# Optimization experiments

Measured on AMD Instinct MI355X. Metric: run time of the kernel, lower is better.

The kernel has to match this reference:

```python
import jax, jax.numpy as jnp
import numpy as np

B, T, NI, NH, NO = 32, 2048, 1, 512, 1


def setup_inputs() -> dict:
    key = jax.random.key(0)
    ks = jax.random.split(key, 7)
    x = jax.random.normal(ks[0], (B, T, NI), dtype=jnp.float32)
    # torch code draws h_0 ~ U[-1,1) once and tiles over batch; here per-batch uniform
    h_0 = jax.random.uniform(ks[1], (B, NH), dtype=jnp.float32) * 2.0 - 1.0
    w_input_std = 1.0 / np.sqrt(NH)
    W_ih = jax.random.normal(ks[2], (NH, NI), dtype=jnp.float32) * w_input_std
    prob_c = 0.1
    w_hidden_std = 1.5 / np.sqrt(prob_c * NH)
    mask = jax.random.bernoulli(ks[3], prob_c, (NH, NH)).astype(jnp.float32)
    W_hh = jax.random.normal(ks[4], (NH, NH), dtype=jnp.float32) * w_hidden_std * mask
    W_hz = jax.random.normal(ks[5], (NO, NH), dtype=jnp.float32) * w_input_std
    W_zh = jax.random.uniform(ks[6], (NH, NO), dtype=jnp.float32, minval=-1.0, maxval=1.0)
    return {"x": x, "h_0": h_0, "W_ih": W_ih, "W_hh": W_hh, "W_hz": W_hz, "W_zh": W_zh}


def reference(x, h_0, W_ih, W_hh, W_hz, W_zh):
    dt, tau = 0.001, 0.01
    alpha = dt / tau  # 0.1
    # precompute input projection for all timesteps: [T, B, NH]
    x_proj = jnp.einsum('bti,hi->tbh', x, W_ih)

    def step(carry, xp_t):
        h_prev, z_prev = carry  # [B,NH], [B,NO]
        h_transfer = jnp.tanh(h_prev)
        dhdt = -h_prev + h_transfer @ W_hh.T + xp_t + z_prev @ W_zh.T
        h_t = h_prev + alpha * dhdt
        z_t = jnp.tanh(h_t) @ W_hz.T
        return (h_t, z_t), (h_t, z_t)

    z0 = jnp.tanh(h_0) @ W_hz.T
    _, (h, z) = jax.lax.scan(step, (h_0, z0), x_proj)
    # scan stacks time first -> [T,B,*]; transpose to [B,T,*]
    return jnp.swapaxes(z, 0, 1), jnp.swapaxes(h, 0, 1)
```

## Files before the change

kernel.cpp:

```cpp
#include <hip/hip_runtime.h>


#define NH   512
#define TT   2048
#define BB   32
#define PAD  96
#define SENT 64

__global__ __launch_bounds__(512) void count_nnz(
    const float* __restrict__ Whh, int* __restrict__ nnz) {
  const int wib  = threadIdx.x >> 6;
  const int lane = threadIdx.x & 63;
  const int row  = blockIdx.x * 8 + wib;
  const float* wrow = Whh + (size_t)row * NH;
  int cnt = 0;
  for (int c = 0; c < NH / 64; ++c)
    cnt += __popcll(__ballot(wrow[c * 64 + lane] != 0.0f));
  if (lane == 0) nnz[row] = cnt;
}

__global__ __launch_bounds__(512) void sort_rows(
    const int* __restrict__ nnz, int* __restrict__ perm) {
  __shared__ int nl[NH];
  const int j = threadIdx.x;
  const int my = nnz[j];
  nl[j] = my;
  __syncthreads();
  int r = 0;
  const int4* p4 = (const int4*)nl;
  for (int i = 0; i < NH / 4; ++i) {
    int4 v = p4[i];
    const int base = i * 4;
    r += (v.x > my) || (v.x == my && base + 0 < j);
    r += (v.y > my) || (v.y == my && base + 1 < j);
    r += (v.z > my) || (v.z == my && base + 2 < j);
    r += (v.w > my) || (v.w == my && base + 3 < j);
  }
  perm[r] = j;
}

__global__ __launch_bounds__(64) void build_schedule(
    const float* __restrict__ Whh, const int* __restrict__ perm,
    float* __restrict__ vals, unsigned* __restrict__ offs,
    int* __restrict__ cntw) {
  __shared__ int claim[2][32];
  const int lane = threadIdx.x;
  const int wid  = blockIdx.x;
  const int p    = wid * 64 + lane;
  const int half = lane >> 5;
  const int home = lane & 31;
  const int row  = perm[p];
  const float* wrow = Whh + (size_t)row * NH;

  unsigned occ32[16];
  int remaining = 0;
  unsigned nonempty = 0;
  #pragma unroll
  for (int r = 0; r < 16; ++r) {
    unsigned lo = 0, hi = 0;
    #pragma unroll
    for (int m = 0; m < 16; ++m) {
      lo |= (wrow[(2 * r)     + 32 * m] != 0.f) ? (1u << m) : 0u;
      hi |= (wrow[(2 * r + 1) + 32 * m] != 0.f) ? (1u << m) : 0u;
    }
    occ32[r] = lo | (hi << 16);
    remaining += __popc(lo) + __popc(hi);
    if (lo) nonempty |= 1u << (2 * r);
    if (hi) nonempty |= 1u << (2 * r + 1);
  }

  int s = 0;
  while (__ballot(remaining > 0) != 0ull) {
    claim[half][home] = SENT;
    __builtin_amdgcn_wave_barrier();

    const bool force = (remaining > 0) && ((PAD - s) <= remaining);
    bool placed = false;
    int  mybank = 0;
    unsigned excl = 0;

    for (int round = 0; round < 8; ++round) {
      unsigned cand = (placed || remaining == 0) ? 0u : (nonempty & ~excl);
      bool want = cand != 0u;
      int bl = 0;
      if (want) {
        unsigned rot = home ? ((cand >> home) | (cand << (32 - home))) : cand;
        bl = (home + __ffs(rot) - 1) & 31;
      }
      if (__ballot(want) == 0ull) break;
      bool win = false;
      if (want) {
        if (force) {
          win = true;
        } else {
          atomicMin(&claim[half][bl], lane);
          __builtin_amdgcn_wave_barrier();
          int c = ((volatile int*)claim[half])[bl];
          if (c == lane) { win = true; ((volatile int*)claim[half])[bl] = -1; }
          else           excl |= 1u << bl;
        }
      }
      __builtin_amdgcn_wave_barrier();
      if (win) { placed = true; mybank = bl; }
    }

    float v = 0.f; unsigned col = 0u;
    if (placed) {
      #pragma unroll
      for (int r = 0; r < 16; ++r) {
        if (r == (mybank >> 1)) {
          unsigned w   = occ32[r];
          unsigned m16 = (mybank & 1) ? (w >> 16) : (w & 0xFFFFu);
          int m = __ffs(m16) - 1;
          col = (unsigned)(mybank + 32 * m);
          unsigned nm = m16 & (m16 - 1u);
          occ32[r] = (mybank & 1) ? ((w & 0x0000FFFFu) | (nm << 16))
                                  : ((w & 0xFFFF0000u) | nm);
          if (nm == 0u) nonempty &= ~(1u << mybank);
        }
      }
      v = wrow[col];
      --remaining;
    }
    vals[s * NH + p] = v;
    offs[s * NH + p] = col;
    ++s;
  }
  if (lane == 0) cntw[wid] = s;
  for (int e = s; e < PAD; ++e) {
    vals[e * NH + p] = 0.f;
    offs[e * NH + p] = 0u;
  }
}

template <int CTRL, int RM>
__device__ __forceinline__ float dppadd(float v) {
  int t = __builtin_amdgcn_update_dpp(0, __float_as_int(v), CTRL, RM, 0xF, true);
  return v + __int_as_float(t);
}
__device__ __forceinline__ float wave_sum_lane63(float v) {
  v = dppadd<0xB1,  0xF>(v);
  v = dppadd<0x4E,  0xF>(v);
  v = dppadd<0x141, 0xF>(v);
  v = dppadd<0x140, 0xF>(v);
  v = dppadd<0x142, 0xA>(v);
  v = dppadd<0x143, 0xC>(v);
  return v;
}

#define ESN_STEP(T_RD, T_WR, RWR, SIDX)                                      \
  {                                                                          \
    float d0 = 0.f, d1 = 0.f, d2 = 0.f, d3 = 0.f;                            \
    _Pragma("unroll")                                                        \
    for (int e = 0; e < PAD; e += 8) {                                       \
      if (e < cw) {                                                          \
        d0 = fmaf(wval[e + 0], T_RD[cidx[e + 0]], d0);                       \
        d1 = fmaf(wval[e + 1], T_RD[cidx[e + 1]], d1);                       \
        d2 = fmaf(wval[e + 2], T_RD[cidx[e + 2]], d2);                       \
        d3 = fmaf(wval[e + 3], T_RD[cidx[e + 3]], d3);                       \
        d0 = fmaf(wval[e + 4], T_RD[cidx[e + 4]], d0);                       \
        d1 = fmaf(wval[e + 5], T_RD[cidx[e + 5]], d1);                       \
        d2 = fmaf(wval[e + 6], T_RD[cidx[e + 6]], d2);                       \
        d3 = fmaf(wval[e + 7], T_RD[cidx[e + 7]], d3);                       \
      }                                                                      \
    }                                                                        \
    float dot  = (d0 + d1) + (d2 + d3);                                      \
    float xp   = x_lds[SIDX] * w_ih;                                         \
    float dhdt = ((dot - h) + xp) + z_prev * w_zh;                           \
    float hn   = h + 0.1f * dhdt;                                            \
    float thn  = tanhf(hn);                                                  \
    T_WR[row] = thn;                                                         \
    oh[(SIDX) * NH + row] = hn;                                              \
    float pzs = wave_sum_lane63(thn * w_hz);                                 \
    if (lane == 63) red[RWR][wid] = pzs;                                     \
    asm volatile("s_waitcnt lgkmcnt(0)\n\ts_barrier" ::: "memory");          \
    float4 r0 = *(const float4*)&red[RWR][0];                                \
    float4 r1 = *(const float4*)&red[RWR][4];                                \
    float z = ((r0.x + r0.y) + (r0.z + r0.w)) + ((r1.x + r1.y) + (r1.z + r1.w)); \
    if (p == 0) oz[SIDX] = z;                                                \
    z_prev = z; h = hn;                                                      \
  }

__global__ __launch_bounds__(512, 2) void esn_steps(
    const float* __restrict__ x,   const float* __restrict__ h0,
    const float* __restrict__ Wih, const float* __restrict__ Whz,
    const float* __restrict__ Wzh, const float* __restrict__ vals,
    const unsigned* __restrict__ offs, const int* __restrict__ perm,
    const int* __restrict__ cntw, float* __restrict__ out) {
  __shared__ float t_lds[2][NH];
  __shared__ float x_lds[TT];
  __shared__ __align__(16) float red[2][8];

  const int p    = threadIdx.x;
  const int b    = blockIdx.x;
  const int lane = p & 63;
  const int wid  = p >> 6;
  const int row  = perm[p];

  float* t0 = t_lds[0];
  float* t1 = t_lds[1];

  for (int i = p; i < TT; i += NH) x_lds[i] = x[(size_t)b * TT + i];

  int cw = __builtin_amdgcn_readfirstlane((cntw[wid] + 7) & ~7);

  float    wval[PAD];
  unsigned cidx[PAD];
  #pragma unroll
  for (int e = 0; e < PAD; ++e) wval[e] = vals[e * NH + p];
  #pragma unroll
  for (int e = 0; e < PAD; ++e) cidx[e] = offs[e * NH + p];

  const float w_ih = Wih[row];
  const float w_hz = Whz[row];
  const float w_zh = Wzh[row];
  float h = h0[(size_t)b * NH + row];

  float* oz = out + (size_t)b * TT;
  float* oh = out + (size_t)BB * TT + (size_t)b * TT * NH;

  float th0 = tanhf(h);
  t0[row] = th0;
  float pz = wave_sum_lane63(th0 * w_hz);
  if (lane == 63) red[0][wid] = pz;
  __syncthreads();
  float4 i0 = *(const float4*)&red[0][0];
  float4 i1 = *(const float4*)&red[0][4];
  float z_prev = ((i0.x + i0.y) + (i0.z + i0.w)) + ((i1.x + i1.y) + (i1.z + i1.w));

  for (int s = 0; s < TT; s += 2) {
    ESN_STEP(t0, t1, 1, s);
    ESN_STEP(t1, t0, 0, s + 1);
  }
}

extern "C" void kernel_launch(void* const* d_in, const int* in_sizes, int n_in,
                              void* d_out, int out_size, void* d_ws,
                              size_t ws_size, hipStream_t stream) {
  const float* x   = (const float*)d_in[0];
  const float* h0  = (const float*)d_in[1];
  const float* Wih = (const float*)d_in[2];
  const float* Whh = (const float*)d_in[3];
  const float* Whz = (const float*)d_in[4];
  const float* Wzh = (const float*)d_in[5];
  float* out = (float*)d_out;

  float*    vals = (float*)d_ws;
  unsigned* offs = (unsigned*)(vals + PAD * NH);
  int*      nnz  = (int*)(offs + PAD * NH);
  int*      perm = nnz + NH;
  int*      cntw = perm + NH;

  hipLaunchKernelGGL(count_nnz, dim3(NH / 8), dim3(512), 0, stream, Whh, nnz);
  hipLaunchKernelGGL(sort_rows, dim3(1), dim3(512), 0, stream, nnz, perm);
  hipLaunchKernelGGL(build_schedule, dim3(8), dim3(64), 0, stream,
                     Whh, perm, vals, offs, cntw);
  hipLaunchKernelGGL(esn_steps, dim3(BB), dim3(512), 0, stream,
                     x, h0, Wih, Whz, Wzh, vals, offs, perm, cntw, out);
}
```

Baseline: 2.846 ms.

## Rework bank-conflict slot scheduler, use fast tanh, byte offsets, and pin registers

The slot-assignment loop that packs sparse W_hh entries into bank-conflict-free columns now uses atomicMax with a priority key favouring lanes with the most remaining entries, allows more rounds, and bounds the outer loop by PAD. The forced placement is also moved after the rounds. In the recurrent step, tanhf is replaced by an exp/rcp-based approximation, and LDS gather indices are precomputed as byte offsets so no shift is needed per access. Empty asm constraints pin the first 80 weight/index pairs in VGPRs to stop the compiler spilling or rematerialising them. The fast tanh gives up some accuracy, and the bounded scheduler loop could drop entries if it fails to place them all.

```diff
diff --git a/kernel.cpp b/kernel.cpp
--- a/kernel.cpp
+++ b/kernel.cpp
@@ -5,7 +5,7 @@
 #define TT   2048
 #define BB   32
 #define PAD  96
-#define SENT 64
+#define PIN  80
 
 __global__ __launch_bounds__(512) void count_nnz(
     const float* __restrict__ Whh, int* __restrict__ nnz) {
@@ -70,16 +70,16 @@
   }
 
   int s = 0;
-  while (__ballot(remaining > 0) != 0ull) {
-    claim[half][home] = SENT;
+  while (__ballot(remaining > 0) != 0ull && s < PAD) {
+    claim[half][home] = 0;
     __builtin_amdgcn_wave_barrier();
 
-    const bool force = (remaining > 0) && ((PAD - s) <= remaining);
     bool placed = false;
     int  mybank = 0;
     unsigned excl = 0;
-
-    for (int round = 0; round < 8; ++round) {
+    const int key = (remaining << 8) | (lane + 1);
+
+    for (int round = 0; round < 12; ++round) {
       unsigned cand = (placed || remaining == 0) ? 0u : (nonempty & ~excl);
       bool want = cand != 0u;
       int bl = 0;
@@ -88,20 +88,23 @@
         bl = (home + __ffs(rot) - 1) & 31;
       }
       if (__ballot(want) == 0ull) break;
-      bool win = false;
+      if (want) atomicMax(&claim[half][bl], key);
+      __builtin_amdgcn_wave_barrier();
       if (want) {
-        if (force) {
-          win = true;
+        int c = ((volatile int*)claim[half])[bl];
+        if (c == key) {
+          placed = true; mybank = bl;
+          ((volatile int*)claim[half])[bl] = 0x7FFFFFFF;
         } else {
-          atomicMin(&claim[half][bl], lane);
-          __builtin_amdgcn_wave_barrier();
-          int c = ((volatile int*)claim[half])[bl];
-          if (c == lane) { win = true; ((volatile int*)claim[half])[bl] = -1; }
-          else           excl |= 1u << bl;
+          excl |= 1u << bl;
         }
       }
       __builtin_amdgcn_wave_barrier();
-      if (win) { placed = true; mybank = bl; }
+    }
+
+    if (!placed && remaining > 0 && (PAD - s) <= remaining) {
+      placed = true;
+      mybank = __ffs(nonempty) - 1;
     }
 
     float v = 0.f; unsigned col = 0u;
@@ -148,27 +151,35 @@
   return v;
 }
 
+__device__ __forceinline__ float ftanh(float x) {
+  float xc = fminf(9.0f, fmaxf(-9.0f, x));
+  float t  = __expf(2.0f * xc);
+  return (t - 1.0f) * __builtin_amdgcn_rcpf(t + 1.0f);
+}
+
+#define GA(T_RD, E) (*(const float*)((const char*)(T_RD) + cidx[E]))
+
 #define ESN_STEP(T_RD, T_WR, RWR, SIDX)                                      \
   {                                                                          \
     float d0 = 0.f, d1 = 0.f, d2 = 0.f, d3 = 0.f;                            \
     _Pragma("unroll")                                                        \
     for (int e = 0; e < PAD; e += 8) {                                       \
       if (e < cw) {                                                          \
-        d0 = fmaf(wval[e + 0], T_RD[cidx[e + 0]], d0);                       \
-        d1 = fmaf(wval[e + 1], T_RD[cidx[e + 1]], d1);                       \
-        d2 = fmaf(wval[e + 2], T_RD[cidx[e + 2]], d2);                       \
-        d3 = fmaf(wval[e + 3], T_RD[cidx[e + 3]], d3);                       \
-        d0 = fmaf(wval[e + 4], T_RD[cidx[e + 4]], d0);                       \
-        d1 = fmaf(wval[e + 5], T_RD[cidx[e + 5]], d1);                       \
-        d2 = fmaf(wval[e + 6], T_RD[cidx[e + 6]], d2);                       \
-        d3 = fmaf(wval[e + 7], T_RD[cidx[e + 7]], d3);                       \
+        d0 = fmaf(wval[e + 0], GA(T_RD, e + 0), d0);                         \
+        d1 = fmaf(wval[e + 1], GA(T_RD, e + 1), d1);                         \
+        d2 = fmaf(wval[e + 2], GA(T_RD, e + 2), d2);                         \
+        d3 = fmaf(wval[e + 3], GA(T_RD, e + 3), d3);                         \
+        d0 = fmaf(wval[e + 4], GA(T_RD, e + 4), d0);                         \
+        d1 = fmaf(wval[e + 5], GA(T_RD, e + 5), d1);                         \
+        d2 = fmaf(wval[e + 6], GA(T_RD, e + 6), d2);                         \
+        d3 = fmaf(wval[e + 7], GA(T_RD, e + 7), d3);                         \
       }                                                                      \
     }                                                                        \
     float dot  = (d0 + d1) + (d2 + d3);                                      \
     float xp   = x_lds[SIDX] * w_ih;                                         \
     float dhdt = ((dot - h) + xp) + z_prev * w_zh;                           \
     float hn   = h + 0.1f * dhdt;                                            \
-    float thn  = tanhf(hn);                                                  \
+    float thn  = ftanh(hn);                                                  \
     T_WR[row] = thn;                                                         \
     oh[(SIDX) * NH + row] = hn;                                              \
     float pzs = wave_sum_lane63(thn * w_hz);                                 \
@@ -207,9 +218,13 @@
   float    wval[PAD];
   unsigned cidx[PAD];
   #pragma unroll
-  for (int e = 0; e < PAD; ++e) wval[e] = vals[e * NH + p];
+  for (int e = 0; e < PAD; ++e) {
+    wval[e] = vals[e * NH + p];
+    cidx[e] = offs[e * NH + p] * 4u;
+  }
   #pragma unroll
-  for (int e = 0; e < PAD; ++e) cidx[e] = offs[e * NH + p];
+  for (int e = 0; e < PIN; ++e)
+    asm volatile("" : "+v"(wval[e]), "+v"(cidx[e]));
 
   const float w_ih = Wih[row];
   const float w_hz = Whz[row];
@@ -219,7 +234,7 @@
   float* oz = out + (size_t)b * TT;
   float* oh = out + (size_t)BB * TT + (size_t)b * TT * NH;
 
-  float th0 = tanhf(h);
+  float th0 = ftanh(h);
   t0[row] = th0;
   float pz = wave_sum_lane63(th0 * w_hz);
   if (lane == 63) red[0][wid] = pz;
```

New measurement: 2.640 ms. 1.08x faster.
